# Optimization experiments

Hardware: AMD Instinct MI355X
Metric: run time of the kernel (lower is better)

Reference implementation:

```python
import jax, jax.numpy as jnp
import numpy as np

H = 4  # heads


def _tconv(x, src, dst, ea, Wq, bq, Wk, bk, Wv, bv, We, Ws, bs):
    # PyG TransformerConv, heads=4, concat=False, root_weight=True, beta=False
    N = x.shape[0]
    Dh = Wq.shape[1] // H  # per-head dim (= hidden_channels)
    q = (x @ Wq + bq).reshape(N, H, Dh)
    k = (x @ Wk + bk).reshape(N, H, Dh)
    v = (x @ Wv + bv).reshape(N, H, Dh)
    e = (ea @ We).reshape(-1, H, Dh)      # lin_edge has no bias in PyG
    kj = k[src] + e                        # [E, H, Dh]
    vj = v[src] + e                        # [E, H, Dh]
    alpha = (q[dst] * kj).sum(-1) / jnp.sqrt(jnp.asarray(Dh, x.dtype))  # [E, H]
    # segment softmax over incoming edges of each dst node
    m = jax.ops.segment_max(alpha, dst, num_segments=N)
    a = jnp.exp(alpha - m[dst])
    s = jax.ops.segment_sum(a, dst, num_segments=N)
    a = a / (s[dst] + 1e-16)
    out = jax.ops.segment_sum(a[:, :, None] * vj, dst, num_segments=N)  # [N, H, Dh]
    out = out.mean(axis=1)                 # concat=False -> mean over heads
    return out + x @ Ws + bs               # root/skip connection


def setup_inputs() -> dict:
    key = jax.random.key(0)
    ks = jax.random.split(key, 32)
    N, E, C_in, C_e, Ch = 50000, 800000, 32, 16, 32
    d = {}
    d['x'] = jax.random.normal(ks[0], (N, C_in), dtype=jnp.float32)
    d['edge_attr'] = jax.random.normal(ks[1], (E, C_e), dtype=jnp.float32)
    d['edge_index'] = jax.random.randint(ks[2], (2, E), 0, N, dtype=jnp.int32)
    s = 0.05
    i = 3
    for L, cin in ((1, C_in), (2, Ch)):
        d[f'Wq{L}'] = jax.random.normal(ks[i], (cin, H * Ch)) * s; i += 1
        d[f'bq{L}'] = jnp.zeros((H * Ch,), jnp.float32)
        d[f'Wk{L}'] = jax.random.normal(ks[i], (cin, H * Ch)) * s; i += 1
        d[f'bk{L}'] = jnp.zeros((H * Ch,), jnp.float32)
        d[f'Wv{L}'] = jax.random.normal(ks[i], (cin, H * Ch)) * s; i += 1
        d[f'bv{L}'] = jnp.zeros((H * Ch,), jnp.float32)
        d[f'We{L}'] = jax.random.normal(ks[i], (C_e, H * Ch)) * s; i += 1
        d[f'Ws{L}'] = jax.random.normal(ks[i], (cin, Ch)) * s; i += 1
        d[f'bs{L}'] = jnp.zeros((Ch,), jnp.float32)
    d['Wm1'] = jax.random.normal(ks[i], (2 * Ch + C_e, Ch)) * s; i += 1
    d['bm1'] = jnp.zeros((Ch,), jnp.float32)
    d['Wm2'] = jax.random.normal(ks[i], (Ch, 1)) * s; i += 1
    d['bm2'] = jnp.zeros((1,), jnp.float32)
    return d


def reference(x, edge_attr, edge_index,
              Wq1, bq1, Wk1, bk1, Wv1, bv1, We1, Ws1, bs1,
              Wq2, bq2, Wk2, bk2, Wv2, bv2, We2, Ws2, bs2,
              Wm1, bm1, Wm2, bm2):
    src, dst = edge_index[0], edge_index[1]
    h = jax.nn.relu(_tconv(x, src, dst, edge_attr, Wq1, bq1, Wk1, bk1, Wv1, bv1, We1, Ws1, bs1))
    h = jax.nn.relu(_tconv(h, src, dst, edge_attr, Wq2, bq2, Wk2, bk2, Wv2, bv2, We2, Ws2, bs2))
    ef = jnp.concatenate([h[src], edge_attr, h[dst]], axis=-1)  # [E, 2*Ch + C_e]
    out = jax.nn.relu(ef @ Wm1 + bm1) @ Wm2 + bm2
    return out.reshape(-1)
```

## Files before the change

### kernel.cpp

```cpp
#include <hip/hip_runtime.h>
#include <hip/hip_fp16.h>
#include <math.h>

#define D128 128
#define CH32 32
#define CE16 16

__global__ void k_hist(const int* __restrict__ dst, int* __restrict__ deg, int E) {
    int e = blockIdx.x * blockDim.x + threadIdx.x;
    if (e < E) atomicAdd(&deg[dst[e]], 1);
}

__global__ void k_scan1(const int* __restrict__ deg, int* __restrict__ offs,
                        int* __restrict__ bsum, int N) {
    __shared__ int buf[256];
    int t = threadIdx.x;
    int i = blockIdx.x * 256 + t;
    int v = (i < N) ? deg[i] : 0;
    buf[t] = v;
    __syncthreads();
    #pragma unroll
    for (int off = 1; off < 256; off <<= 1) {
        int val = (t >= off) ? buf[t - off] : 0;
        __syncthreads();
        buf[t] += val;
        __syncthreads();
    }
    if (i < N) offs[i] = buf[t] - v;
    if (t == 255) bsum[blockIdx.x] = buf[255];
}

__global__ void k_scan2(const int* __restrict__ bsum, int* __restrict__ boff, int nb) {
    __shared__ int buf[256];
    int t = threadIdx.x;
    int v = (t < nb) ? bsum[t] : 0;
    buf[t] = v;
    __syncthreads();
    #pragma unroll
    for (int off = 1; off < 256; off <<= 1) {
        int val = (t >= off) ? buf[t - off] : 0;
        __syncthreads();
        buf[t] += val;
        __syncthreads();
    }
    if (t < nb) boff[t] = buf[t] - v;
}

__global__ void k_scan3(const int* __restrict__ boff, int* __restrict__ offs,
                        int* __restrict__ cur, int N, int E) {
    int i = blockIdx.x * blockDim.x + threadIdx.x;
    if (i < N) {
        int o = offs[i] + boff[i >> 8];
        offs[i] = o;
        cur[i] = o;
    }
    if (i == 0) offs[N] = E;
}

__global__ void k_scatter_idx(const int* __restrict__ src, const int* __restrict__ dst,
                              int* __restrict__ cur, int* __restrict__ csr_srcb,
                              int2* __restrict__ csr_de, int E) {
    int e = blockIdx.x * blockDim.x + threadIdx.x;
    if (e < E) {
        int d = dst[e];
        int p = atomicAdd(&cur[d], 1);
        csr_srcb[p] = src[e] << 9;
        csr_de[p] = make_int2(d, e);
    }
}

__global__ __launch_bounds__(256) void k_gather_ea(
    const float4* __restrict__ ea4, const int2* __restrict__ csr_de,
    __half* __restrict__ ea_h, int E) {
    int idx = blockIdx.x * 256 + threadIdx.x;
    int p = idx >> 2, q = idx & 3;
    if (p < E) {
        int e = csr_de[p].y;
        float4 v = ea4[e * 4 + q];
        union { __half2 h[2]; float2 f; } u;
        u.h[0] = __floats2half2_rn(v.x, v.y);
        u.h[1] = __floats2half2_rn(v.z, v.w);
        *(float2*)(ea_h + (size_t)p * 16 + q * 4) = u.f;
    }
}

__global__ void k_wqe(const float* __restrict__ Wq1, const float* __restrict__ bq1,
                      const float* __restrict__ We1,
                      const float* __restrict__ Wq2, const float* __restrict__ bq2,
                      const float* __restrict__ We2,
                      float* __restrict__ Wqe1, float* __restrict__ bqe1,
                      float* __restrict__ Wqe2, float* __restrict__ bqe2) {
    int t = threadIdx.x, h = t >> 4, j = t & 15;
    const float QS = 0.17677669529663687f * 1.4426950408889634f;
    int b = blockIdx.x;
    int layer = (b >= 33);
    int i = layer ? b - 33 : b;
    const float* Wq = layer ? Wq2 : Wq1;
    const float* bq = layer ? bq2 : bq1;
    const float* We = layer ? We2 : We1;
    float* Wqe = layer ? Wqe2 : Wqe1;
    float* bqe = layer ? bqe2 : bqe1;
    const float* base = (i < 32) ? (Wq + i * D128) : bq;
    float s = 0.f;
    #pragma unroll
    for (int d = 0; d < 32; d++)
        s = fmaf(base[h * 32 + d], We[j * D128 + h * 32 + d], s);
    s *= QS;
    if (i < 32) Wqe[i * 64 + t] = s;
    else        bqe[t] = s;
}

__global__ __launch_bounds__(128) void k_nodeproj(
    const float* __restrict__ xin,
    const float* __restrict__ Wq, const float* __restrict__ bq,
    const float* __restrict__ Wk, const float* __restrict__ bk,
    const float* __restrict__ Wv, const float* __restrict__ bv,
    const float* __restrict__ Ws, const float* __restrict__ bs,
    const float* __restrict__ Wqe, const float* __restrict__ bqe,
    __half* __restrict__ qh, __half* __restrict__ kvh,
    float* __restrict__ skip, float* __restrict__ qeb, int N)
{
    int tid = threadIdx.x;
    int c   = tid & 31;
    int pos = ((tid >> 2) << 3) | (tid & 3);
    float wq[32], wk[32], wv[32], ws[32];
    #pragma unroll
    for (int j = 0; j < 32; j++) {
        wq[j] = Wq[j * D128 + tid];
        wk[j] = Wk[j * D128 + tid];
        wv[j] = Wv[j * D128 + tid];
        ws[j] = Ws[j * CH32 + c];
    }
    float bqc = bq[tid], bkc = bk[tid], bvc = bv[tid], bsc = bs[c];
    __shared__ float wqeS[32][64];
    __shared__ float xs[4][32];
    for (int i = tid; i < 2048; i += 128) wqeS[i >> 6][i & 63] = Wqe[i];
    float bqec = bqe[tid & 63];
    int nchunk = (N + 3) / 4;
    for (int chk = blockIdx.x; chk < nchunk; chk += gridDim.x) {
        int base = chk * 4;
        {
            int r = tid >> 5;
            int n = base + r;
            xs[r][c] = (n < N) ? xin[n * 32 + c] : 0.f;
        }
        __syncthreads();
        #pragma unroll
        for (int r = 0; r < 4; r++) {
            int n = base + r;
            if (n < N) {
                float aq = bqc, ak = bkc, av = bvc;
                #pragma unroll
                for (int j = 0; j < 32; j++) {
                    float xj = xs[r][j];
                    aq = fmaf(xj, wq[j], aq);
                    ak = fmaf(xj, wk[j], ak);
                    av = fmaf(xj, wv[j], av);
                }
                qh[(size_t)n * D128 + tid]     = __float2half_rn(aq);
                kvh[(size_t)n * 256 + pos]     = __float2half_rn(ak);
                kvh[(size_t)n * 256 + pos + 4] = __float2half_rn(av);
            }
        }
        {
            int r = tid >> 5;
            int n = base + r;
            if (n < N) {
                float as = bsc;
                #pragma unroll
                for (int j = 0; j < 32; j++) as = fmaf(xs[r][j], ws[j], as);
                skip[n * 32 + c] = as;
            }
        }
        {
            int c6 = tid & 63;
            int r0 = (tid >> 6) << 1;
            #pragma unroll
            for (int rr = 0; rr < 2; rr++) {
                int n = base + r0 + rr;
                if (n < N) {
                    float a = bqec;
                    #pragma unroll
                    for (int j = 0; j < 32; j++)
                        a = fmaf(xs[r0 + rr][j], wqeS[j][c6], a);
                    qeb[(size_t)n * 64 + c6] = a;
                }
            }
        }
        __syncthreads();
    }
}

__global__ __launch_bounds__(64) void k_edgeattn(
    const __half* __restrict__ qh, const __half* __restrict__ kvh,
    const float* __restrict__ skip,
    const __half* __restrict__ ea_csr, const float* __restrict__ We,
    const int* __restrict__ offs, const int* __restrict__ csr_srcb,
    const float* __restrict__ qeb, float* __restrict__ hout)
{
    int node = blockIdx.x;
    int lane = threadIdx.x;
    int eg   = lane >> 5;
    int c    = lane & 31;
    int g    = c & 7;
    int c4   = c << 2;

    const float QS = 0.17677669529663687f * 1.4426950408889634f;
    float2 qraw = *(const float2*)&qh[(size_t)node * D128 + c4];
    float2 q01 = __half22float2(*(const __half2*)&qraw.x);
    float2 q23 = __half22float2(*(const __half2*)&qraw.y);
    float4 qv = make_float4(q01.x * QS, q01.y * QS, q23.x * QS, q23.y * QS);

    float2 qe01 = *(const float2*)&qeb[(size_t)node * 64 + ((c >> 3) << 4) + 2 * g];
    float qe0 = qe01.x, qe1 = qe01.y;

    int s0 = offs[node], s1 = offs[node + 1];
    int deg = s1 - s0;

    float l = 0.f;
    float ac0 = 0.f, ac1 = 0.f, ac2 = 0.f, ac3 = 0.f;
    float se0 = 0.f, se1 = 0.f;

    if (deg > 0) {
        int last = s1 - 1;
        const char* kvb = (const char*)kvh;
        const char* eab = (const char*)ea_csr;
        int toff = c << 4;
        int goff = g << 2;

        auto eidx = [&](int p) { return min(s0 + 2 * p + eg, last); };
        auto ldidx = [&](int p) { return csr_srcb[eidx(p)]; };
        auto ldkv  = [&](int ib) {
            return *(const float4*)(kvb + (size_t)(unsigned)ib + toff);
        };
        auto ldea  = [&](int p) {
            return *(const __half2*)(eab + ((size_t)eidx(p) << 5) + goff);
        };
        auto pair = [&](const float4& kvr, const __half2& eah, int p) {
            bool valid = (s0 + 2 * p + eg) <= last;
            float2 k01 = __half22float2(*(const __half2*)&kvr.x);
            float2 k23 = __half22float2(*(const __half2*)&kvr.y);
            float2 v01 = __half22float2(*(const __half2*)&kvr.z);
            float2 v23 = __half22float2(*(const __half2*)&kvr.w);
            float2 eav = __half22float2(eah);
            float t = fmaf(qv.y, k01.y, qv.x * k01.x);
            t = fmaf(qv.z, k23.x, t);
            t = fmaf(qv.w, k23.y, t);
            t = fmaf(qe0, eav.x, t);
            t = fmaf(qe1, eav.y, t);
            t += __shfl_xor(t, 1);
            t += __shfl_xor(t, 2);
            t += __shfl_xor(t, 4);
            float pp = valid ? __builtin_amdgcn_exp2f(t) : 0.f;
            l += pp;
            ac0 = fmaf(pp, v01.x, ac0);
            ac1 = fmaf(pp, v01.y, ac1);
            ac2 = fmaf(pp, v23.x, ac2);
            ac3 = fmaf(pp, v23.y, ac3);
            se0 = fmaf(pp, eav.x, se0);
            se1 = fmaf(pp, eav.y, se1);
        };

        int iA0 = ldidx(0), iA1 = ldidx(1);
        int iB0 = ldidx(2), iB1 = ldidx(3);
        float4 kA0 = ldkv(iA0), kA1 = ldkv(iA1);
        __half2 eA0 = ldea(0),  eA1 = ldea(1);

        int p = 0;
        int nIter = (deg + 7) >> 3;
        for (int it = 0; it < nIter; ++it) {
            float4 kB0 = ldkv(iB0), kB1 = ldkv(iB1);
            __half2 eB0 = ldea(p + 2), eB1 = ldea(p + 3);
            iA0 = ldidx(p + 4); iA1 = ldidx(p + 5);

            pair(kA0, eA0, p + 0);
            pair(kA1, eA1, p + 1);

            kA0 = ldkv(iA0); kA1 = ldkv(iA1);
            eA0 = ldea(p + 4); eA1 = ldea(p + 5);
            iB0 = ldidx(p + 6); iB1 = ldidx(p + 7);

            pair(kB0, eB0, p + 2);
            pair(kB1, eB1, p + 3);

            p += 4;
        }
    }

    l   += __shfl_xor(l, 32);
    ac0 += __shfl_xor(ac0, 32);
    ac1 += __shfl_xor(ac1, 32);
    ac2 += __shfl_xor(ac2, 32);
    ac3 += __shfl_xor(ac3, 32);
    se0 += __shfl_xor(se0, 32);
    se1 += __shfl_xor(se1, 32);

    float inv = 1.0f / (l + 1e-16f);
    float r0 = ac0 * inv, r1 = ac1 * inv, r2 = ac2 * inv, r3 = ac3 * inv;
    float sn0 = se0 * inv, sn1 = se1 * inv;

    int gb = lane & ~7;
    #pragma unroll
    for (int j = 0; j < 16; j++) {
        float sj = __shfl((j & 1) ? sn1 : sn0, gb | (j >> 1), 64);
        float4 wj = *(const float4*)&We[j * D128 + c4];
        r0 = fmaf(sj, wj.x, r0);
        r1 = fmaf(sj, wj.y, r1);
        r2 = fmaf(sj, wj.z, r2);
        r3 = fmaf(sj, wj.w, r3);
    }
    r0 += __shfl_xor(r0, 8);  r0 += __shfl_xor(r0, 16);
    r1 += __shfl_xor(r1, 8);  r1 += __shfl_xor(r1, 16);
    r2 += __shfl_xor(r2, 8);  r2 += __shfl_xor(r2, 16);
    r3 += __shfl_xor(r3, 8);  r3 += __shfl_xor(r3, 16);
    if (lane < 8) {
        const float4 sk = *(const float4*)&skip[(size_t)node * 32 + c4];
        float4 o;
        o.x = fmaxf(fmaf(0.25f, r0, sk.x), 0.f);
        o.y = fmaxf(fmaf(0.25f, r1, sk.y), 0.f);
        o.z = fmaxf(fmaf(0.25f, r2, sk.z), 0.f);
        o.w = fmaxf(fmaf(0.25f, r3, sk.w), 0.f);
        *(float4*)&hout[(size_t)node * 32 + c4] = o;
    }
}

__global__ __launch_bounds__(256) void k_postproj(
    const float* __restrict__ h, const float* __restrict__ Wm1,
    const float* __restrict__ bm1, __half* __restrict__ hA,
    __half* __restrict__ hC, int N) {
    __shared__ float WA[32][32], WC[32][32];
    __shared__ float hs[8][32];
    int tid = threadIdx.x;
    for (int i = tid; i < 1024; i += 256) {
        WA[i >> 5][i & 31] = Wm1[i];
        WC[i >> 5][i & 31] = Wm1[48 * 32 + i];
    }
    int col = tid & 31, r = tid >> 5;
    float bb = bm1[col];
    __syncthreads();
    int nchunk = (N + 7) / 8;
    for (int chk = blockIdx.x; chk < nchunk; chk += gridDim.x) {
        int n = chk * 8 + r;
        hs[r][col] = (n < N) ? h[(size_t)n * 32 + col] : 0.f;
        __syncthreads();
        if (n < N) {
            float a = bb, cc = 0.f;
            #pragma unroll
            for (int j = 0; j < 32; j++) {
                float hj = hs[r][j];
                a  = fmaf(hj, WA[j][col], a);
                cc = fmaf(hj, WC[j][col], cc);
            }
            hA[(size_t)n * 32 + col] = __float2half_rn(a);
            hC[(size_t)n * 32 + col] = __float2half_rn(cc);
        }
        __syncthreads();
    }
}

__global__ __launch_bounds__(256) void k_mlp(
    const __half* __restrict__ hA, const __half* __restrict__ hC,
    const __half* __restrict__ ea_csr,
    const int* __restrict__ csr_srcb, const int2* __restrict__ csr_de,
    const float* __restrict__ Wm1, const float* __restrict__ Wm2,
    const float* __restrict__ bm2, float* __restrict__ out, int E)
{
    __shared__ float4 B4[16 * 8];
    __shared__ float wm2L[32];
    int tid = threadIdx.x;
    const float4* Wm1B = (const float4*)(Wm1 + 32 * 32);
    for (int i = tid; i < 128; i += 256) B4[i] = Wm1B[i];
    if (tid < 32) wm2L[tid] = Wm2[tid];
    __syncthreads();

    int p = blockIdx.x * 256 + tid;
    if (p >= E) return;
    float b2 = bm2[0];
    int srcb = csr_srcb[p];
    int2 de  = csr_de[p];

    const float4* pa = (const float4*)((const char*)hA + ((size_t)(unsigned)srcb >> 3));
    const float4* pc = (const float4*)((const char*)hC + (size_t)de.x * 64);
    const float4* ev = (const float4*)(ea_csr + (size_t)p * 16);

    float zc[32];
    #pragma unroll
    for (int i = 0; i < 4; i++) {
        float4 ra = pa[i], rc = pc[i];
        const __half2* ha = (const __half2*)&ra;
        const __half2* hc = (const __half2*)&rc;
        #pragma unroll
        for (int k = 0; k < 4; k++) {
            float2 fa = __half22float2(ha[k]);
            float2 fc = __half22float2(hc[k]);
            zc[i * 8 + k * 2 + 0] = fa.x + fc.x;
            zc[i * 8 + k * 2 + 1] = fa.y + fc.y;
        }
    }

    auto dorow = [&](int j, float xj) {
        #pragma unroll
        for (int c4 = 0; c4 < 8; c4++) {
            float4 w = B4[j * 8 + c4];
            zc[c4 * 4 + 0] = fmaf(xj, w.x, zc[c4 * 4 + 0]);
            zc[c4 * 4 + 1] = fmaf(xj, w.y, zc[c4 * 4 + 1]);
            zc[c4 * 4 + 2] = fmaf(xj, w.z, zc[c4 * 4 + 2]);
            zc[c4 * 4 + 3] = fmaf(xj, w.w, zc[c4 * 4 + 3]);
        }
    };

    float4 raw0 = ev[0], raw1 = ev[1];
    const __half2* hp0 = (const __half2*)&raw0;
    const __half2* hp1 = (const __half2*)&raw1;
    #pragma unroll
    for (int k = 0; k < 4; k++) {
        float2 ef = __half22float2(hp0[k]);
        dorow(2 * k + 0, ef.x);
        dorow(2 * k + 1, ef.y);
    }
    #pragma unroll
    for (int k = 0; k < 4; k++) {
        float2 ef = __half22float2(hp1[k]);
        dorow(8 + 2 * k + 0, ef.x);
        dorow(8 + 2 * k + 1, ef.y);
    }

    float y = b2;
    #pragma unroll
    for (int c = 0; c < 32; c++) y += fmaxf(zc[c], 0.f) * wm2L[c];
    out[de.y] = y;
}

extern "C" void kernel_launch(void* const* d_in, const int* in_sizes, int n_in,
                              void* d_out, int out_size, void* d_ws, size_t ws_size,
                              hipStream_t stream)
{
    const float* x  = (const float*)d_in[0];
    const float* ea = (const float*)d_in[1];
    const int*   ei = (const int*)d_in[2];
    const int N = in_sizes[0] / 32;
    const int E = in_sizes[1] / 16;
    const int* src = ei;
    const int* dst = ei + E;

    const float *Wq1 = (const float*)d_in[3],  *bq1 = (const float*)d_in[4];
    const float *Wk1 = (const float*)d_in[5],  *bk1 = (const float*)d_in[6];
    const float *Wv1 = (const float*)d_in[7],  *bv1 = (const float*)d_in[8];
    const float *We1 = (const float*)d_in[9],  *Ws1 = (const float*)d_in[10];
    const float *bs1 = (const float*)d_in[11];
    const float *Wq2 = (const float*)d_in[12], *bq2 = (const float*)d_in[13];
    const float *Wk2 = (const float*)d_in[14], *bk2 = (const float*)d_in[15];
    const float *Wv2 = (const float*)d_in[16], *bv2 = (const float*)d_in[17];
    const float *We2 = (const float*)d_in[18], *Ws2 = (const float*)d_in[19];
    const float *bs2 = (const float*)d_in[20];
    const float *Wm1 = (const float*)d_in[21], *bm1 = (const float*)d_in[22];
    const float *Wm2 = (const float*)d_in[23], *bm2 = (const float*)d_in[24];

    char* w = (char*)d_ws;
    auto alloc = [&](size_t bytes) -> void* {
        void* p = (void*)w;
        w += (bytes + 255) & ~(size_t)255;
        return p;
    };
    int* deg      = (int*)alloc((size_t)N * 4);
    int* offs     = (int*)alloc(((size_t)N + 1) * 4);
    int* cur      = (int*)alloc((size_t)N * 4);
    int* bsum     = (int*)alloc(256 * 4);
    int* boff     = (int*)alloc(256 * 4);
    int* csr_srcb = (int*)alloc((size_t)E * 4);
    int2* csr_de  = (int2*)alloc((size_t)E * 8);
    __half* ea_csr= (__half*)alloc((size_t)E * 16 * 2);
    __half* qhb   = (__half*)alloc((size_t)N * 128 * 2);
    __half* kvb   = (__half*)alloc((size_t)N * 256 * 2);
    float* skipb  = (float*)alloc((size_t)N * 32 * 4);
    float* h1     = (float*)alloc((size_t)N * 32 * 4);
    float* h2     = (float*)alloc((size_t)N * 32 * 4);
    float* Wqe1   = (float*)alloc(32 * 64 * 4);
    float* bqe1   = (float*)alloc(64 * 4);
    float* Wqe2   = (float*)alloc(32 * 64 * 4);
    float* bqe2   = (float*)alloc(64 * 4);
    float* qeb    = (float*)alloc((size_t)N * 64 * 4);
    __half* hA    = (__half*)alloc((size_t)N * 32 * 2);
    __half* hC    = (__half*)alloc((size_t)N * 32 * 2);

    hipMemsetAsync(deg, 0, (size_t)N * 4, stream);

    int ebl = (E + 255) / 256;
    int nb  = (N + 255) / 256;
    k_wqe<<<66, 64, 0, stream>>>(Wq1, bq1, We1, Wq2, bq2, We2,
                                 Wqe1, bqe1, Wqe2, bqe2);
    k_hist<<<ebl, 256, 0, stream>>>(dst, deg, E);
    k_scan1<<<nb, 256, 0, stream>>>(deg, offs, bsum, N);
    k_scan2<<<1, 256, 0, stream>>>(bsum, boff, nb);
    k_scan3<<<nb, 256, 0, stream>>>(boff, offs, cur, N, E);
    k_scatter_idx<<<ebl, 256, 0, stream>>>(src, dst, cur, csr_srcb, csr_de, E);
    k_gather_ea<<<(E * 4 + 255) / 256, 256, 0, stream>>>(
        (const float4*)ea, csr_de, ea_csr, E);

    k_nodeproj<<<1024, 128, 0, stream>>>(x, Wq1, bq1, Wk1, bk1, Wv1, bv1, Ws1, bs1,
                                         Wqe1, bqe1, qhb, kvb, skipb, qeb, N);
    k_edgeattn<<<N, 64, 0, stream>>>(qhb, kvb, skipb, ea_csr, We1,
                                     offs, csr_srcb, qeb, h1);
    k_nodeproj<<<1024, 128, 0, stream>>>(h1, Wq2, bq2, Wk2, bk2, Wv2, bv2, Ws2, bs2,
                                         Wqe2, bqe2, qhb, kvb, skipb, qeb, N);
    k_edgeattn<<<N, 64, 0, stream>>>(qhb, kvb, skipb, ea_csr, We2,
                                     offs, csr_srcb, qeb, h2);
    k_postproj<<<1024, 256, 0, stream>>>(h2, Wm1, bm1, hA, hC, N);
    k_mlp<<<ebl, 256, 0, stream>>>(hA, hC, ea_csr, csr_srcb, csr_de,
                                   Wm1, Wm2, bm2, (float*)d_out, E);
}
```

Measured before the change: 511.0 us.

## Fuse small kernels: init with histogram, nodeproj with ea gather, postproj into edgeattn

Merges the Wqe precompute and degree histogram into one launch, runs the edge-attribute gather as extra blocks of the first node projection launch, and folds the post-projection (hA/hC) into the second edge-attention kernel's epilogue using shuffles. This removes three kernel launches and the h2 round trip through global memory. In exchange, the epilogue reads Wm1 from global memory per node and does a 32-step shuffle reduction in every block.

```diff
diff --git a/kernel.cpp b/kernel.cpp
--- a/kernel.cpp
+++ b/kernel.cpp
@@ -6,9 +6,41 @@
 #define CH32 32
 #define CE16 16
 
-__global__ void k_hist(const int* __restrict__ dst, int* __restrict__ deg, int E) {
-    int e = blockIdx.x * blockDim.x + threadIdx.x;
-    if (e < E) atomicAdd(&deg[dst[e]], 1);
+__global__ __launch_bounds__(256) void k_init(
+    const float* __restrict__ Wq1, const float* __restrict__ bq1,
+    const float* __restrict__ We1,
+    const float* __restrict__ Wq2, const float* __restrict__ bq2,
+    const float* __restrict__ We2,
+    float* __restrict__ Wqe1, float* __restrict__ bqe1,
+    float* __restrict__ Wqe2, float* __restrict__ bqe2,
+    const int* __restrict__ dst, int* __restrict__ deg, int E)
+{
+    if (blockIdx.x < 66) {
+        int t = threadIdx.x;
+        if (t < 64) {
+            int h = t >> 4, j = t & 15;
+            const float QS = 0.17677669529663687f * 1.4426950408889634f;
+            int b = blockIdx.x;
+            int layer = (b >= 33);
+            int i = layer ? b - 33 : b;
+            const float* Wq = layer ? Wq2 : Wq1;
+            const float* bq = layer ? bq2 : bq1;
+            const float* We = layer ? We2 : We1;
+            float* Wqe = layer ? Wqe2 : Wqe1;
+            float* bqe = layer ? bqe2 : bqe1;
+            const float* base = (i < 32) ? (Wq + i * D128) : bq;
+            float s = 0.f;
+            #pragma unroll
+            for (int d = 0; d < 32; d++)
+                s = fmaf(base[h * 32 + d], We[j * D128 + h * 32 + d], s);
+            s *= QS;
+            if (i < 32) Wqe[i * 64 + t] = s;
+            else        bqe[t] = s;
+        }
+    } else {
+        int e = (blockIdx.x - 66) * 256 + threadIdx.x;
+        if (e < E) atomicAdd(&deg[dst[e]], 1);
+    }
 }
 
 __global__ void k_scan1(const int* __restrict__ deg, int* __restrict__ offs,
@@ -69,48 +101,7 @@
     }
 }
 
-__global__ __launch_bounds__(256) void k_gather_ea(
-    const float4* __restrict__ ea4, const int2* __restrict__ csr_de,
-    __half* __restrict__ ea_h, int E) {
-    int idx = blockIdx.x * 256 + threadIdx.x;
-    int p = idx >> 2, q = idx & 3;
-    if (p < E) {
-        int e = csr_de[p].y;
-        float4 v = ea4[e * 4 + q];
-        union { __half2 h[2]; float2 f; } u;
-        u.h[0] = __floats2half2_rn(v.x, v.y);
-        u.h[1] = __floats2half2_rn(v.z, v.w);
-        *(float2*)(ea_h + (size_t)p * 16 + q * 4) = u.f;
-    }
-}
-
-__global__ void k_wqe(const float* __restrict__ Wq1, const float* __restrict__ bq1,
-                      const float* __restrict__ We1,
-                      const float* __restrict__ Wq2, const float* __restrict__ bq2,
-                      const float* __restrict__ We2,
-                      float* __restrict__ Wqe1, float* __restrict__ bqe1,
-                      float* __restrict__ Wqe2, float* __restrict__ bqe2) {
-    int t = threadIdx.x, h = t >> 4, j = t & 15;
-    const float QS = 0.17677669529663687f * 1.4426950408889634f;
-    int b = blockIdx.x;
-    int layer = (b >= 33);
-    int i = layer ? b - 33 : b;
-    const float* Wq = layer ? Wq2 : Wq1;
-    const float* bq = layer ? bq2 : bq1;
-    const float* We = layer ? We2 : We1;
-    float* Wqe = layer ? Wqe2 : Wqe1;
-    float* bqe = layer ? bqe2 : bqe1;
-    const float* base = (i < 32) ? (Wq + i * D128) : bq;
-    float s = 0.f;
-    #pragma unroll
-    for (int d = 0; d < 32; d++)
-        s = fmaf(base[h * 32 + d], We[j * D128 + h * 32 + d], s);
-    s *= QS;
-    if (i < 32) Wqe[i * 64 + t] = s;
-    else        bqe[t] = s;
-}
-
-__global__ __launch_bounds__(128) void k_nodeproj(
+__device__ __forceinline__ void nodeproj_body(
     const float* __restrict__ xin,
     const float* __restrict__ Wq, const float* __restrict__ bq,
     const float* __restrict__ Wk, const float* __restrict__ bk,
@@ -118,7 +109,8 @@
     const float* __restrict__ Ws, const float* __restrict__ bs,
     const float* __restrict__ Wqe, const float* __restrict__ bqe,
     __half* __restrict__ qh, __half* __restrict__ kvh,
-    float* __restrict__ skip, float* __restrict__ qeb, int N)
+    float* __restrict__ skip, float* __restrict__ qeb, int N,
+    int bid, int nblocks)
 {
     int tid = threadIdx.x;
     int c   = tid & 31;
@@ -137,7 +129,7 @@
     for (int i = tid; i < 2048; i += 128) wqeS[i >> 6][i & 63] = Wqe[i];
     float bqec = bqe[tid & 63];
     int nchunk = (N + 3) / 4;
-    for (int chk = blockIdx.x; chk < nchunk; chk += gridDim.x) {
+    for (int chk = bid; chk < nchunk; chk += nblocks) {
         int base = chk * 4;
         {
             int r = tid >> 5;
@@ -191,12 +183,62 @@
     }
 }
 
+__global__ __launch_bounds__(128) void k_nodeproj(
+    const float* __restrict__ xin,
+    const float* __restrict__ Wq, const float* __restrict__ bq,
+    const float* __restrict__ Wk, const float* __restrict__ bk,
+    const float* __restrict__ Wv, const float* __restrict__ bv,
+    const float* __restrict__ Ws, const float* __restrict__ bs,
+    const float* __restrict__ Wqe, const float* __restrict__ bqe,
+    __half* __restrict__ qh, __half* __restrict__ kvh,
+    float* __restrict__ skip, float* __restrict__ qeb, int N)
+{
+    nodeproj_body(xin, Wq, bq, Wk, bk, Wv, bv, Ws, bs, Wqe, bqe,
+                  qh, kvh, skip, qeb, N, blockIdx.x, gridDim.x);
+}
+
+__global__ __launch_bounds__(128) void k_np_gea(
+    const float* __restrict__ xin,
+    const float* __restrict__ Wq, const float* __restrict__ bq,
+    const float* __restrict__ Wk, const float* __restrict__ bk,
+    const float* __restrict__ Wv, const float* __restrict__ bv,
+    const float* __restrict__ Ws, const float* __restrict__ bs,
+    const float* __restrict__ Wqe, const float* __restrict__ bqe,
+    __half* __restrict__ qh, __half* __restrict__ kvh,
+    float* __restrict__ skip, float* __restrict__ qeb, int N,
+    const float4* __restrict__ ea4, const int2* __restrict__ csr_de,
+    __half* __restrict__ ea_h, int E)
+{
+    if (blockIdx.x < 1024) {
+        nodeproj_body(xin, Wq, bq, Wk, bk, Wv, bv, Ws, bs, Wqe, bqe,
+                      qh, kvh, skip, qeb, N, blockIdx.x, 1024);
+    } else {
+        int base = (blockIdx.x - 1024) * 256 + threadIdx.x;
+        #pragma unroll
+        for (int s = 0; s < 2; s++) {
+            int idx = base + s * 128;
+            int p = idx >> 2, q = idx & 3;
+            if (p < E) {
+                int e = csr_de[p].y;
+                float4 v = ea4[e * 4 + q];
+                union { __half2 h[2]; float2 f; } u;
+                u.h[0] = __floats2half2_rn(v.x, v.y);
+                u.h[1] = __floats2half2_rn(v.z, v.w);
+                *(float2*)(ea_h + (size_t)p * 16 + q * 4) = u.f;
+            }
+        }
+    }
+}
+
+template<int PP>
 __global__ __launch_bounds__(64) void k_edgeattn(
     const __half* __restrict__ qh, const __half* __restrict__ kvh,
     const float* __restrict__ skip,
     const __half* __restrict__ ea_csr, const float* __restrict__ We,
     const int* __restrict__ offs, const int* __restrict__ csr_srcb,
-    const float* __restrict__ qeb, float* __restrict__ hout)
+    const float* __restrict__ qeb, float* __restrict__ hout,
+    const float* __restrict__ Wm1, const float* __restrict__ bm1,
+    __half* __restrict__ hA, __half* __restrict__ hC)
 {
     int node = blockIdx.x;
     int lane = threadIdx.x;
@@ -313,48 +355,41 @@
     r1 += __shfl_xor(r1, 8);  r1 += __shfl_xor(r1, 16);
     r2 += __shfl_xor(r2, 8);  r2 += __shfl_xor(r2, 16);
     r3 += __shfl_xor(r3, 8);  r3 += __shfl_xor(r3, 16);
-    if (lane < 8) {
-        const float4 sk = *(const float4*)&skip[(size_t)node * 32 + c4];
+
+    if constexpr (PP == 0) {
+        if (lane < 8) {
+            const float4 sk = *(const float4*)&skip[(size_t)node * 32 + c4];
+            float4 o;
+            o.x = fmaxf(fmaf(0.25f, r0, sk.x), 0.f);
+            o.y = fmaxf(fmaf(0.25f, r1, sk.y), 0.f);
+            o.z = fmaxf(fmaf(0.25f, r2, sk.z), 0.f);
+            o.w = fmaxf(fmaf(0.25f, r3, sk.w), 0.f);
+            *(float4*)&hout[(size_t)node * 32 + c4] = o;
+        }
+    } else {
+        int a8 = (c & 7) << 2;
+        const float4 sk = *(const float4*)&skip[(size_t)node * 32 + a8];
         float4 o;
         o.x = fmaxf(fmaf(0.25f, r0, sk.x), 0.f);
         o.y = fmaxf(fmaf(0.25f, r1, sk.y), 0.f);
         o.z = fmaxf(fmaf(0.25f, r2, sk.z), 0.f);
         o.w = fmaxf(fmaf(0.25f, r3, sk.w), 0.f);
-        *(float4*)&hout[(size_t)node * 32 + c4] = o;
-    }
-}
-
-__global__ __launch_bounds__(256) void k_postproj(
-    const float* __restrict__ h, const float* __restrict__ Wm1,
-    const float* __restrict__ bm1, __half* __restrict__ hA,
-    __half* __restrict__ hC, int N) {
-    __shared__ float WA[32][32], WC[32][32];
-    __shared__ float hs[8][32];
-    int tid = threadIdx.x;
-    for (int i = tid; i < 1024; i += 256) {
-        WA[i >> 5][i & 31] = Wm1[i];
-        WC[i >> 5][i & 31] = Wm1[48 * 32 + i];
-    }
-    int col = tid & 31, r = tid >> 5;
-    float bb = bm1[col];
-    __syncthreads();
-    int nchunk = (N + 7) / 8;
-    for (int chk = blockIdx.x; chk < nchunk; chk += gridDim.x) {
-        int n = chk * 8 + r;
-        hs[r][col] = (n < N) ? h[(size_t)n * 32 + col] : 0.f;
-        __syncthreads();
-        if (n < N) {
-            float a = bb, cc = 0.f;
-            #pragma unroll
-            for (int j = 0; j < 32; j++) {
-                float hj = hs[r][j];
-                a  = fmaf(hj, WA[j][col], a);
-                cc = fmaf(hj, WC[j][col], cc);
-            }
-            hA[(size_t)n * 32 + col] = __float2half_rn(a);
-            hC[(size_t)n * 32 + col] = __float2half_rn(cc);
-        }
-        __syncthreads();
+        int col = lane & 31;
+        const float* Wb = (lane < 32) ? (Wm1 + col) : (Wm1 + 48 * 32 + col);
+        float acc = (lane < 32) ? bm1[col] : 0.f;
+        #pragma unroll
+        for (int a = 0; a < 8; a++) {
+            float hx = __shfl(o.x, a, 64);
+            float hy = __shfl(o.y, a, 64);
+            float hz = __shfl(o.z, a, 64);
+            float hw = __shfl(o.w, a, 64);
+            acc = fmaf(hx, Wb[(4 * a + 0) * 32], acc);
+            acc = fmaf(hy, Wb[(4 * a + 1) * 32], acc);
+            acc = fmaf(hz, Wb[(4 * a + 2) * 32], acc);
+            acc = fmaf(hw, Wb[(4 * a + 3) * 32], acc);
+        }
+        __half* dstp = (lane < 32) ? hA : hC;
+        dstp[(size_t)node * 32 + col] = __float2half_rn(acc);
     }
 }
 
@@ -474,7 +509,6 @@
     __half* kvb   = (__half*)alloc((size_t)N * 256 * 2);
     float* skipb  = (float*)alloc((size_t)N * 32 * 4);
     float* h1     = (float*)alloc((size_t)N * 32 * 4);
-    float* h2     = (float*)alloc((size_t)N * 32 * 4);
     float* Wqe1   = (float*)alloc(32 * 64 * 4);
     float* bqe1   = (float*)alloc(64 * 4);
     float* Wqe2   = (float*)alloc(32 * 64 * 4);
@@ -487,25 +521,26 @@
 
     int ebl = (E + 255) / 256;
     int nb  = (N + 255) / 256;
-    k_wqe<<<66, 64, 0, stream>>>(Wq1, bq1, We1, Wq2, bq2, We2,
-                                 Wqe1, bqe1, Wqe2, bqe2);
-    k_hist<<<ebl, 256, 0, stream>>>(dst, deg, E);
+    int gb  = (E * 4 + 255) / 256;
+
+    k_init<<<66 + ebl, 256, 0, stream>>>(Wq1, bq1, We1, Wq2, bq2, We2,
+                                         Wqe1, bqe1, Wqe2, bqe2, dst, deg, E);
     k_scan1<<<nb, 256, 0, stream>>>(deg, offs, bsum, N);
     k_scan2<<<1, 256, 0, stream>>>(bsum, boff, nb);
     k_scan3<<<nb, 256, 0, stream>>>(boff, offs, cur, N, E);
     k_scatter_idx<<<ebl, 256, 0, stream>>>(src, dst, cur, csr_srcb, csr_de, E);
-    k_gather_ea<<<(E * 4 + 255) / 256, 256, 0, stream>>>(
-        (const float4*)ea, csr_de, ea_csr, E);
-
-    k_nodeproj<<<1024, 128, 0, stream>>>(x, Wq1, bq1, Wk1, bk1, Wv1, bv1, Ws1, bs1,
-                                         Wqe1, bqe1, qhb, kvb, skipb, qeb, N);
-    k_edgeattn<<<N, 64, 0, stream>>>(qhb, kvb, skipb, ea_csr, We1,
-                                     offs, csr_srcb, qeb, h1);
+
+    k_np_gea<<<1024 + gb, 128, 0, stream>>>(
+        x, Wq1, bq1, Wk1, bk1, Wv1, bv1, Ws1, bs1, Wqe1, bqe1,
+        qhb, kvb, skipb, qeb, N, (const float4*)ea, csr_de, ea_csr, E);
+    k_edgeattn<0><<<N, 64, 0, stream>>>(qhb, kvb, skipb, ea_csr, We1,
+                                        offs, csr_srcb, qeb, h1,
+                                        Wm1, bm1, hA, hC);
     k_nodeproj<<<1024, 128, 0, stream>>>(h1, Wq2, bq2, Wk2, bk2, Wv2, bv2, Ws2, bs2,
                                          Wqe2, bqe2, qhb, kvb, skipb, qeb, N);
-    k_edgeattn<<<N, 64, 0, stream>>>(qhb, kvb, skipb, ea_csr, We2,
-                                     offs, csr_srcb, qeb, h2);
-    k_postproj<<<1024, 256, 0, stream>>>(h2, Wm1, bm1, hA, hC, N);
+    k_edgeattn<1><<<N, 64, 0, stream>>>(qhb, kvb, skipb, ea_csr, We2,
+                                        offs, csr_srcb, qeb, h1,
+                                        Wm1, bm1, hA, hC);
     k_mlp<<<ebl, 256, 0, stream>>>(hA, hC, ea_csr, csr_srcb, csr_de,
                                    Wm1, Wm2, bm2, (float*)d_out, E);
 }
```

After: 508.5 us. No clear change (-0.5%).
